# Kernel optimization log

Measured on AMD Instinct MI355X. Metric: run time of the kernel, lower is better.

The kernel has to match this reference:

```python
import jax, jax.numpy as jnp
import numpy as np

N = 4096          # nodes
F_IN = 1386       # txt_feat_len
NHID = 1024       # per-head hidden
NHEADS = 8
CODE = 64         # code_len
LRELU_ALPHA = 0.2
NEG_INF = -9e15


def _build_adj(x):
    # F.normalize + cosine sim, threshold 0.8, sign -> {0,1}, then symmetric D^-1/2 A D^-1/2
    norm = jnp.maximum(jnp.linalg.norm(x, axis=1, keepdims=True), 1e-12)
    xn = x / norm
    sim = xn @ xn.T                                  # (N,N)
    A = (sim >= 0.8).astype(x.dtype)                 # sign after thresholding
    rowsum = A.sum(axis=1)
    r = jnp.where(rowsum > 0, rowsum ** -0.5, 0.0)
    adj = r[:, None] * A * r[None, :]                # symmetric normalized
    return jax.lax.stop_gradient(adj)                # torch code detaches x / adj is non-diff


def _gat_head(x, W, a, adj, concat):
    # x: (N,Fin), W: (Fin,H), a: (2H,1)
    H = W.shape[1]
    Wh = x @ W                                        # (N,H)
    f1 = Wh @ a[:H]                                   # (N,1)
    f2 = Wh @ a[H:]                                   # (N,1)
    e = jax.nn.leaky_relu(f1 + f2.T, LRELU_ALPHA)     # (N,N) pairwise scores
    e = jnp.where(adj > 0, e, NEG_INF)
    att = jax.nn.softmax(e, axis=1)                   # masked softmax (dropout off: eval)
    h = att @ Wh                                      # (N,H)
    return jax.nn.elu(h) if concat else h


def setup_inputs() -> dict:
    key = jax.random.key(0)
    k = jax.random.split(key, 5)
    x = jax.random.normal(k[0], (N, F_IN), dtype=jnp.float32)
    s_in = 1.0 / np.sqrt(F_IN)
    W_att = jax.random.uniform(k[1], (NHEADS, F_IN, NHID), jnp.float32, -s_in, s_in)
    a_att = jax.random.uniform(k[2], (NHEADS, 2 * NHID, 1), jnp.float32, -0.1, 0.1)
    s_h = 1.0 / np.sqrt(NHEADS * NHID)
    W_out = jax.random.uniform(k[3], (NHEADS * NHID, CODE), jnp.float32, -s_h, s_h)
    a_out = jax.random.uniform(k[4], (2 * CODE, 1), jnp.float32, -0.1, 0.1)
    return {"x": x, "W_att": W_att, "a_att": a_att, "W_out": W_out, "a_out": a_out}


def reference(x, W_att, a_att, W_out, a_out):
    adj = _build_adj(x)
    # 8 concat heads, vmapped over the head axis
    heads = jax.vmap(lambda W, a: _gat_head(x, W, a, adj, True))(W_att, a_att)  # (8,N,NHID)
    h = jnp.transpose(heads, (1, 0, 2)).reshape(N, NHEADS * NHID)               # cat dim=1
    out = _gat_head(h, W_out, a_out, adj, False)                                # (N,CODE)
    code = jnp.tanh(1.0 * out)                                                   # alpha=1.0
    return code
```

## Files before the change

### kernel.cpp

```cpp
#include <hip/hip_runtime.h>
#include <hip/hip_bf16.h>
#include <stdint.h>
#include <math.h>


typedef __bf16 bf16x8 __attribute__((ext_vector_type(8)));
typedef float  f32x4  __attribute__((ext_vector_type(4)));
typedef unsigned short ushort8 __attribute__((ext_vector_type(8)));

#define AS1C(p) ((const __attribute__((address_space(1))) void*)(p))
#define AS3(p)  ((__attribute__((address_space(3))) void*)(p))

#define MODE_BF16 0
#define MODE_SIM  1
#define MODE_F32  2

__device__ __forceinline__ float bfbits2f(unsigned short u) {
    return __uint_as_float(((unsigned)u) << 16);
}
__device__ __forceinline__ unsigned short f2bfbits(float v) {
    __hip_bfloat16 b = __float2bfloat16(v);
    return *(unsigned short*)&b;
}

template<int MODE>
__device__ __forceinline__ void gemm_body(
    __hip_bfloat16* __restrict__ As, __hip_bfloat16* __restrict__ Bs,
    int bx, int by,
    const __hip_bfloat16* __restrict__ A,
    const __hip_bfloat16* __restrict__ B,
    int lda, int ldb, int K,
    void* __restrict__ Cv, int ldc, int Nreal,
    const float* __restrict__ norms,
    unsigned* __restrict__ mask,
    unsigned* __restrict__ summary)
{
    const int tid  = threadIdx.x;
    const int lane = tid & 63;
    const int wave = tid >> 6;
    const int m0   = bx * 128;
    const int n0   = by * 128;

    f32x4 acc[4][4];
#pragma unroll
    for (int i = 0; i < 4; ++i)
#pragma unroll
        for (int j = 0; j < 4; ++j)
#pragma unroll
            for (int k = 0; k < 4; ++k) acc[i][j][k] = 0.f;

    const int wm = wave >> 1, wn = wave & 1;
    const int q  = lane >> 4, ln = lane & 15;

    const int kIters = K >> 5;
    for (int kt = 0; kt < kIters; ++kt) {
        __syncthreads();
#pragma unroll
        for (int p = 0; p < 2; ++p) {
            const int t   = p * 256 + tid;
            const int row = t >> 2;
            const int kb  = (t & 3) ^ ((t >> 3) & 3);
            const __hip_bfloat16* ga = A + (long long)(m0 + row) * lda + kt * 32 + kb * 8;
            const __hip_bfloat16* gb = B + (long long)(n0 + row) * ldb + kt * 32 + kb * 8;
            __hip_bfloat16* sa = As + (p * 256 + wave * 64) * 8;
            __hip_bfloat16* sb = Bs + (p * 256 + wave * 64) * 8;
            __builtin_amdgcn_global_load_lds(AS1C(ga), AS3(sa), 16, 0, 0);
            __builtin_amdgcn_global_load_lds(AS1C(gb), AS3(sb), 16, 0, 0);
        }
        __syncthreads();

        bf16x8 afr[4], bfr[4];
#pragma unroll
        for (int rg = 0; rg < 4; ++rg) {
            const int r = wm * 64 + rg * 16 + ln;
            const int s = q ^ ((r >> 1) & 3);
            afr[rg] = *(const bf16x8*)(As + r * 32 + s * 8);
        }
#pragma unroll
        for (int cg = 0; cg < 4; ++cg) {
            const int r = wn * 64 + cg * 16 + ln;
            const int s = q ^ ((r >> 1) & 3);
            bfr[cg] = *(const bf16x8*)(Bs + r * 32 + s * 8);
        }
#pragma unroll
        for (int rg = 0; rg < 4; ++rg)
#pragma unroll
            for (int cg = 0; cg < 4; ++cg)
                acc[rg][cg] = __builtin_amdgcn_mfma_f32_16x16x32_bf16(
                    afr[rg], bfr[cg], acc[rg][cg], 0, 0, 0);
    }

#pragma unroll
    for (int rg = 0; rg < 4; ++rg) {
#pragma unroll
        for (int cg = 0; cg < 4; ++cg) {
#pragma unroll
            for (int i = 0; i < 4; ++i) {
                const int row = m0 + wm * 64 + rg * 16 + q * 4 + i;
                const int col = n0 + wn * 64 + cg * 16 + ln;
                const float v = acc[rg][cg][i];
                if (MODE == MODE_BF16) {
                    __hip_bfloat16* C = (__hip_bfloat16*)Cv;
                    C[(long long)row * ldc + col] = __float2bfloat16(v);
                } else if (MODE == MODE_SIM) {
                    if (v >= 0.8f * norms[row] * norms[col]) {
                        atomicOr(&mask[row * 128 + (col >> 5)], 1u << (col & 31));
                        atomicOr(&summary[row * 4 + (col >> 10)], 1u << ((col >> 5) & 31));
                        atomicOr(&mask[col * 128 + (row >> 5)], 1u << (row & 31));
                        atomicOr(&summary[col * 4 + (row >> 10)], 1u << ((row >> 5) & 31));
                    }
                } else {
                    if (col < Nreal) {
                        float* C = (float*)Cv;
                        C[(long long)row * ldc + col] = v;
                    }
                }
            }
        }
    }
}

__global__ __launch_bounds__(256)
void prestage(const float* __restrict__ x,
              const float* __restrict__ W_att,
              const float* __restrict__ W_out,
              const float* __restrict__ a_att,
              __hip_bfloat16* __restrict__ x_bf,
              float* __restrict__ norms,
              __hip_bfloat16* __restrict__ Wt_bf,
              __hip_bfloat16* __restrict__ WoutT,
              float* __restrict__ wa)
{
    __shared__ float ts[32][33];
    __shared__ float red[4];
    const int id  = blockIdx.x;
    const int tid = threadIdx.x;

    if (id < 4096) {
        const int i = id;
        float ss = 0.f;
        for (int c = tid; c < 1408; c += 256) {
            float v = (c < 1386) ? x[(long long)i * 1386 + c] : 0.f;
            x_bf[(long long)i * 1408 + c] = __float2bfloat16(v);
            ss += v * v;
        }
        for (int off = 32; off; off >>= 1) ss += __shfl_down(ss, off);
        if ((tid & 63) == 0) red[tid >> 6] = ss;
        __syncthreads();
        if (tid == 0) norms[i] = fmaxf(sqrtf(red[0] + red[1] + red[2] + red[3]), 1e-12f);
        return;
    }
    if (id < 16384) {
        const float* s; __hip_bfloat16* d;
        int K, N, Kpad, Npad, k0, n0;
        if (id < 15360) {
            const int b = id - 4096;
            const int h = b / 1408, r = b % 1408;
            const int kx = r % 44, ny = r / 44;
            s = W_att + (long long)h * 1386 * 1024;
            d = Wt_bf + (long long)h * 1024 * 1408;
            K = 1386; N = 1024; Kpad = 1408; Npad = 1024;
            k0 = kx * 32; n0 = ny * 32;
        } else {
            const int r = id - 15360;
            s = W_out; d = WoutT;
            K = 8192; N = 64; Kpad = 8192; Npad = 128;
            k0 = (r & 255) * 32; n0 = (r >> 8) * 32;
        }
        const int tx = tid & 31, ty = tid >> 5;
#pragma unroll
        for (int i = 0; i < 4; ++i) {
            const int k = k0 + ty + i * 8;
            const int n = n0 + tx;
            ts[ty + i * 8][tx] = (k < K && n < N) ? s[(long long)k * N + n] : 0.f;
        }
        __syncthreads();
#pragma unroll
        for (int i = 0; i < 4; ++i) {
            const int n  = n0 + ty + i * 8;
            const int kk = k0 + tx;
            if (n < Npad && kk < Kpad)
                d[(long long)n * Kpad + kk] = __float2bfloat16(ts[tx][ty + i * 8]);
        }
        return;
    }
    {
        const int b = id - 16384;
        const int h = b / 352, r = b % 352;
        const int wave = tid >> 6, lane = tid & 63;
        const int c = r * 4 + wave;
        float s1 = 0.f, s2 = 0.f;
        if (c < 1386) {
            const float* wr = W_att + ((long long)h * 1386 + c) * 1024;
            const float* a1 = a_att + (long long)h * 2048;
            const float* a2 = a1 + 1024;
#pragma unroll
            for (int t = 0; t < 16; ++t) {
                const int j = lane + t * 64;
                const float w = wr[j];
                s1 += w * a1[j];
                s2 += w * a2[j];
            }
        }
        for (int off = 32; off; off >>= 1) { s1 += __shfl_down(s1, off); s2 += __shfl_down(s2, off); }
        if (lane == 0) {
            wa[(h * 2 + 0) * 1408 + c] = s1;
            wa[(h * 2 + 1) * 1408 + c] = s2;
        }
    }
}

__global__ __launch_bounds__(256, 2)
void mega_gemm(const __hip_bfloat16* __restrict__ x_bf,
               const __hip_bfloat16* __restrict__ Wt_bf,
               __hip_bfloat16* __restrict__ Wh,
               const float* __restrict__ norms,
               unsigned* __restrict__ mask,
               unsigned* __restrict__ summ,
               const float* __restrict__ x,
               const float* __restrict__ wa,
               float2* __restrict__ f12)
{
    __shared__ __align__(16) __hip_bfloat16 As[128 * 32];
    __shared__ __align__(16) __hip_bfloat16 Bs[128 * 32];
    const int id = blockIdx.x;

    if (id < 528) {
        int t = (int)((sqrtf(8.f * id + 1.f) - 1.f) * 0.5f);
        while (t * (t + 1) / 2 > id) --t;
        while ((t + 1) * (t + 2) / 2 <= id) ++t;
        const int by = t, bx = id - t * (t + 1) / 2;
        gemm_body<MODE_SIM>(As, Bs, bx, by, x_bf, x_bf, 1408, 1408, 1408,
                            nullptr, 0, 0, norms, mask, summ);
        return;
    }
    if (id < 2576) {
        const int b  = id - 528;
        const int z  = b >> 8;
        const int r  = b & 255;
        const int bx = r & 31, by = r >> 5;
        gemm_body<MODE_BF16>(As, Bs, bx, by,
                             x_bf, Wt_bf + (long long)z * 1024 * 1408,
                             1408, 1408, 1408,
                             Wh + (long long)z * 4096 * 1024, 1024, 1024,
                             nullptr, nullptr, nullptr);
        return;
    }
    {
        const int b    = id - 2576;
        const int wave = threadIdx.x >> 6, lane = threadIdx.x & 63;
        const int i    = b * 4 + wave;
        float s[16];
#pragma unroll
        for (int j = 0; j < 16; ++j) s[j] = 0.f;
        const float* xr = x + (long long)i * 1386;
        for (int c = lane; c < 1386; c += 64) {
            const float v = xr[c];
#pragma unroll
            for (int j = 0; j < 16; ++j) s[j] += v * wa[j * 1408 + c];
        }
#pragma unroll
        for (int j = 0; j < 16; ++j)
            for (int off = 32; off; off >>= 1) s[j] += __shfl_down(s[j], off);
        if (lane == 0) {
#pragma unroll
            for (int h = 0; h < 8; ++h)
                f12[(long long)h * 4096 + i] = make_float2(s[h * 2], s[h * 2 + 1]);
        }
    }
}

__global__ __launch_bounds__(256, 2)
void out_gemm(const __hip_bfloat16* __restrict__ hout,
              const __hip_bfloat16* __restrict__ WoutT,
              float* __restrict__ parts)
{
    __shared__ __align__(16) __hip_bfloat16 As[128 * 32];
    __shared__ __align__(16) __hip_bfloat16 Bs[128 * 32];
    const int z = blockIdx.z;
    gemm_body<MODE_F32>(As, Bs, blockIdx.x, 0,
                        hout + z * 512, WoutT + z * 512, 8192, 8192, 512,
                        parts + (long long)z * 4096 * 64, 64, 64,
                        nullptr, nullptr, nullptr);
}

__global__ __launch_bounds__(256)
void attn_head(const __hip_bfloat16* __restrict__ Wh,
               const float2* __restrict__ f12,
               const unsigned* __restrict__ mask,
               const unsigned* __restrict__ summary,
               __hip_bfloat16* __restrict__ hout)
{
    const int wv   = threadIdx.x >> 6;
    const int lane = threadIdx.x & 63;
    const int i    = blockIdx.x * 4 + wv;
    const int h    = blockIdx.y;
    const float2* f = f12 + (long long)h * 4096;
    const float f1 = f[i].x;
    const unsigned* mrow = mask + (long long)i * 128;
    const __hip_bfloat16* WhH = Wh + (long long)h * 4096 * 1024;
    const uint4 sm = *(const uint4*)(summary + (long long)i * 4);
    unsigned sw[4] = { sm.x, sm.y, sm.z, sm.w };
    const int cbase = lane * 16;

    float m = -INFINITY, l = 0.f;
    float acc[16];
#pragma unroll
    for (int k = 0; k < 16; ++k) acc[k] = 0.f;

#pragma unroll
    for (int s = 0; s < 4; ++s) {
        unsigned sb = sw[s];
        while (sb) {
            const int w = s * 32 + __builtin_ctz(sb);
            sb &= sb - 1;
            unsigned bits = mrow[w];
            while (bits) {
                const int j = w * 32 + __builtin_ctz(bits);
                bits &= bits - 1;
                float e = f1 + f[j].y;
                e = e > 0.f ? e : 0.2f * e;
                float wgt;
                if (e > m) {
                    const float sc = __expf(m - e);
                    l *= sc;
#pragma unroll
                    for (int k = 0; k < 16; ++k) acc[k] *= sc;
                    m = e; wgt = 1.f;
                } else {
                    wgt = __expf(e - m);
                }
                l += wgt;
                const ushort8* p = (const ushort8*)(WhH + (long long)j * 1024 + cbase);
                const ushort8 w0 = p[0], w1 = p[1];
#pragma unroll
                for (int k = 0; k < 8; ++k) acc[k]     += wgt * bfbits2f(w0[k]);
#pragma unroll
                for (int k = 0; k < 8; ++k) acc[k + 8] += wgt * bfbits2f(w1[k]);
            }
        }
    }
    const float inv = 1.f / l;
    ushort8 o0, o1;
#pragma unroll
    for (int k = 0; k < 8; ++k) {
        float v = acc[k] * inv;     v = v > 0.f ? v : (__expf(v) - 1.f); o0[k] = f2bfbits(v);
        float u = acc[k + 8] * inv; u = u > 0.f ? u : (__expf(u) - 1.f); o1[k] = f2bfbits(u);
    }
    ushort8* op = (ushort8*)(hout + (long long)i * 8192 + (long long)h * 1024 + cbase);
    op[0] = o0; op[1] = o1;
}

__global__ void out_reduce_f(const float* __restrict__ parts,
                             const float* __restrict__ a_out,
                             float* __restrict__ Cout,
                             float* __restrict__ f1o,
                             float* __restrict__ f2o)
{
    const int i = blockIdx.x, c = threadIdx.x;
    float v = 0.f;
#pragma unroll
    for (int z = 0; z < 16; ++z) v += parts[(long long)z * 4096 * 64 + (long long)i * 64 + c];
    Cout[(long long)i * 64 + c] = v;
    float s1 = v * a_out[c];
    float s2 = v * a_out[64 + c];
    for (int off = 32; off; off >>= 1) { s1 += __shfl_down(s1, off); s2 += __shfl_down(s2, off); }
    if (c == 0) { f1o[i] = s1; f2o[i] = s2; }
}

__global__ __launch_bounds__(256)
void attn_out(const float* __restrict__ Cout,
              const float* __restrict__ f1o,
              const float* __restrict__ f2o,
              const unsigned* __restrict__ mask,
              const unsigned* __restrict__ summary,
              float* __restrict__ out)
{
    const int wv = threadIdx.x >> 6;
    const int c  = threadIdx.x & 63;
    const int i  = blockIdx.x * 4 + wv;
    const float f1 = f1o[i];
    const unsigned* mrow = mask + (long long)i * 128;
    const uint4 sm = *(const uint4*)(summary + (long long)i * 4);
    unsigned sw[4] = { sm.x, sm.y, sm.z, sm.w };
    float m = -INFINITY, l = 0.f, acc = 0.f;
#pragma unroll
    for (int s = 0; s < 4; ++s) {
        unsigned sb = sw[s];
        while (sb) {
            const int w = s * 32 + __builtin_ctz(sb);
            sb &= sb - 1;
            unsigned bits = mrow[w];
            while (bits) {
                const int j = w * 32 + __builtin_ctz(bits);
                bits &= bits - 1;
                float e = f1 + f2o[j];
                e = e > 0.f ? e : 0.2f * e;
                float wgt;
                if (e > m) { const float sc = __expf(m - e); l *= sc; acc *= sc; m = e; wgt = 1.f; }
                else       { wgt = __expf(e - m); }
                l += wgt;
                acc += wgt * Cout[(long long)j * 64 + c];
            }
        }
    }
    out[(long long)i * 64 + c] = tanhf(acc / l);
}

extern "C" void kernel_launch(void* const* d_in, const int* in_sizes, int n_in,
                              void* d_out, int out_size, void* d_ws, size_t ws_size,
                              hipStream_t stream)
{
    (void)in_sizes; (void)n_in; (void)out_size;
    const float* x     = (const float*)d_in[0];
    const float* W_att = (const float*)d_in[1];
    const float* a_att = (const float*)d_in[2];
    const float* W_out = (const float*)d_in[3];
    const float* a_out = (const float*)d_in[4];
    float* out = (float*)d_out;

    char* ws = (char*)d_ws;
    size_t off = 0;
    auto alloc = [&](size_t bytes) -> void* {
        void* p = ws + off;
        off += (bytes + 255) & ~(size_t)255;
        return p;
    };

    __hip_bfloat16* x_bf  = (__hip_bfloat16*)alloc(4096LL * 1408 * 2);
    __hip_bfloat16* Wt_bf = (__hip_bfloat16*)alloc(8LL * 1024 * 1408 * 2);
    __hip_bfloat16* WoutT = (__hip_bfloat16*)alloc(128LL * 8192 * 2);
    float*          norms = (float*)alloc(4096 * 4);
    unsigned*       mask  = (unsigned*)alloc(4096LL * 128 * 4);
    unsigned*       summ  = (unsigned*)alloc(4096LL * 4 * 4);
    float*          wa    = (float*)alloc(16LL * 1408 * 4);
    float2*         f12   = (float2*)alloc(8LL * 4096 * 8);
    float*          parts = (float*)alloc(16LL * 4096 * 64 * 4);
    float*          Cout  = (float*)alloc(4096LL * 64 * 4);
    float*          f1o   = (float*)alloc(4096 * 4);
    float*          f2o   = (float*)alloc(4096 * 4);
    __hip_bfloat16* Wh    = (__hip_bfloat16*)alloc(8LL * 4096 * 1024 * 2);
    __hip_bfloat16* hout  = (__hip_bfloat16*)alloc(8LL * 4096 * 1024 * 2);
    if (off > ws_size) return;

    hipMemsetAsync(mask, 0, 4096LL * 128 * 4 + 4096LL * 4 * 4, stream);

    prestage<<<19200, 256, 0, stream>>>(x, W_att, W_out, a_att,
                                        x_bf, norms, Wt_bf, WoutT, wa);

    mega_gemm<<<3600, 256, 0, stream>>>(x_bf, Wt_bf, Wh, norms, mask, summ,
                                        x, wa, f12);

    attn_head<<<dim3(1024, 8), 256, 0, stream>>>(Wh, f12, mask, summ, hout);

    out_gemm<<<dim3(32, 1, 16), 256, 0, stream>>>(hout, WoutT, parts);

    out_reduce_f<<<4096, 64, 0, stream>>>(parts, a_out, Cout, f1o, f2o);
    attn_out<<<1024, 256, 0, stream>>>(Cout, f1o, f2o, mask, summ, out);
}
```

Before: 326.3 us.

## Fuse ELU into Wh GEMM epilogue for self-loop-only rows and skip attention

Adds a per-row check for whether a node's adjacency holds only its own self-loop. For those rows the masked softmax puts all its weight on the node itself, so the head output is simply ELU(Wh). The Wh GEMM epilogue now writes that directly into hout, and the attention kernel exits early for such rows. This requires splitting the combined GEMM launch so the similarity mask is complete before the Wh GEMM runs, which costs extra launch serialization and per-row mask reads in the epilogue.

```diff
diff --git a/kernel.cpp b/kernel.cpp
--- a/kernel.cpp
+++ b/kernel.cpp
@@ -11,9 +11,9 @@
 #define AS1C(p) ((const __attribute__((address_space(1))) void*)(p))
 #define AS3(p)  ((__attribute__((address_space(3))) void*)(p))
 
-#define MODE_BF16 0
-#define MODE_SIM  1
-#define MODE_F32  2
+#define MODE_WH  0
+#define MODE_SIM 1
+#define MODE_F32 2
 
 __device__ __forceinline__ float bfbits2f(unsigned short u) {
     return __uint_as_float(((unsigned)u) << 16);
@@ -21,6 +21,19 @@
 __device__ __forceinline__ unsigned short f2bfbits(float v) {
     __hip_bfloat16 b = __float2bfloat16(v);
     return *(unsigned short*)&b;
+}
+
+__device__ __forceinline__ bool row_fast(const unsigned* __restrict__ mask,
+                                         const unsigned* __restrict__ summ,
+                                         int row)
+{
+    const uint4 s = *(const uint4*)(summ + row * 4);
+    unsigned sw[4] = { s.x, s.y, s.z, s.w };
+    const int wi = row >> 5;
+    bool fast = (sw[wi >> 5] == (1u << (wi & 31)));
+    sw[wi >> 5] = 0;
+    fast = fast && !(sw[0] | sw[1] | sw[2] | sw[3]);
+    return fast && (mask[row * 128 + wi] == (1u << (row & 31)));
 }
 
 template<int MODE>
@@ -33,7 +46,8 @@
     void* __restrict__ Cv, int ldc, int Nreal,
     const float* __restrict__ norms,
     unsigned* __restrict__ mask,
-    unsigned* __restrict__ summary)
+    unsigned* __restrict__ summary,
+    __hip_bfloat16* __restrict__ hout)
 {
     const int tid  = threadIdx.x;
     const int lane = tid & 63;
@@ -93,15 +107,22 @@
 #pragma unroll
     for (int rg = 0; rg < 4; ++rg) {
 #pragma unroll
-        for (int cg = 0; cg < 4; ++cg) {
-#pragma unroll
-            for (int i = 0; i < 4; ++i) {
-                const int row = m0 + wm * 64 + rg * 16 + q * 4 + i;
+        for (int i = 0; i < 4; ++i) {
+            const int row = m0 + wm * 64 + rg * 16 + q * 4 + i;
+            bool fast = false;
+            if (MODE == MODE_WH) fast = row_fast(mask, summary, row);
+#pragma unroll
+            for (int cg = 0; cg < 4; ++cg) {
                 const int col = n0 + wn * 64 + cg * 16 + ln;
                 const float v = acc[rg][cg][i];
-                if (MODE == MODE_BF16) {
-                    __hip_bfloat16* C = (__hip_bfloat16*)Cv;
-                    C[(long long)row * ldc + col] = __float2bfloat16(v);
+                if (MODE == MODE_WH) {
+                    if (fast) {
+                        const float u = v > 0.f ? v : (__expf(v) - 1.f);
+                        hout[(long long)row * 8192 + col] = __float2bfloat16(u);
+                    } else {
+                        __hip_bfloat16* C = (__hip_bfloat16*)Cv;
+                        C[(long long)row * ldc + col] = __float2bfloat16(v);
+                    }
                 } else if (MODE == MODE_SIM) {
                     if (v >= 0.8f * norms[row] * norms[col]) {
                         atomicOr(&mask[row * 128 + (col >> 5)], 1u << (col & 31));
@@ -211,15 +232,13 @@
 }
 
 __global__ __launch_bounds__(256, 2)
-void mega_gemm(const __hip_bfloat16* __restrict__ x_bf,
-               const __hip_bfloat16* __restrict__ Wt_bf,
-               __hip_bfloat16* __restrict__ Wh,
-               const float* __restrict__ norms,
-               unsigned* __restrict__ mask,
-               unsigned* __restrict__ summ,
-               const float* __restrict__ x,
-               const float* __restrict__ wa,
-               float2* __restrict__ f12)
+void simf12(const __hip_bfloat16* __restrict__ x_bf,
+            const float* __restrict__ norms,
+            unsigned* __restrict__ mask,
+            unsigned* __restrict__ summ,
+            const float* __restrict__ x,
+            const float* __restrict__ wa,
+            float2* __restrict__ f12)
 {
     __shared__ __align__(16) __hip_bfloat16 As[128 * 32];
     __shared__ __align__(16) __hip_bfloat16 Bs[128 * 32];
@@ -231,23 +250,11 @@
         while ((t + 1) * (t + 2) / 2 <= id) ++t;
         const int by = t, bx = id - t * (t + 1) / 2;
         gemm_body<MODE_SIM>(As, Bs, bx, by, x_bf, x_bf, 1408, 1408, 1408,
-                            nullptr, 0, 0, norms, mask, summ);
+                            nullptr, 0, 0, norms, mask, summ, nullptr);
         return;
     }
-    if (id < 2576) {
-        const int b  = id - 528;
-        const int z  = b >> 8;
-        const int r  = b & 255;
-        const int bx = r & 31, by = r >> 5;
-        gemm_body<MODE_BF16>(As, Bs, bx, by,
-                             x_bf, Wt_bf + (long long)z * 1024 * 1408,
-                             1408, 1408, 1408,
-                             Wh + (long long)z * 4096 * 1024, 1024, 1024,
-                             nullptr, nullptr, nullptr);
-        return;
-    }
     {
-        const int b    = id - 2576;
+        const int b    = id - 528;
         const int wave = threadIdx.x >> 6, lane = threadIdx.x & 63;
         const int i    = b * 4 + wave;
         float s[16];
@@ -268,6 +275,27 @@
                 f12[(long long)h * 4096 + i] = make_float2(s[h * 2], s[h * 2 + 1]);
         }
     }
+}
+
+__global__ __launch_bounds__(256, 2)
+void whh(const __hip_bfloat16* __restrict__ x_bf,
+         const __hip_bfloat16* __restrict__ Wt_bf,
+         __hip_bfloat16* __restrict__ Wh,
+         __hip_bfloat16* __restrict__ hout,
+         unsigned* __restrict__ mask,
+         unsigned* __restrict__ summ)
+{
+    __shared__ __align__(16) __hip_bfloat16 As[128 * 32];
+    __shared__ __align__(16) __hip_bfloat16 Bs[128 * 32];
+    const int id = blockIdx.x;
+    const int z  = id >> 8;
+    const int r  = id & 255;
+    const int bx = r & 31, by = r >> 5;
+    gemm_body<MODE_WH>(As, Bs, bx, by,
+                       x_bf, Wt_bf + (long long)z * 1024 * 1408,
+                       1408, 1408, 1408,
+                       Wh + (long long)z * 4096 * 1024, 1024, 1024,
+                       nullptr, mask, summ, hout + (long long)z * 1024);
 }
 
 __global__ __launch_bounds__(256, 2)
@@ -281,20 +309,22 @@
     gemm_body<MODE_F32>(As, Bs, blockIdx.x, 0,
                         hout + z * 512, WoutT + z * 512, 8192, 8192, 512,
                         parts + (long long)z * 4096 * 64, 64, 64,
-                        nullptr, nullptr, nullptr);
+                        nullptr, nullptr, nullptr, nullptr);
 }
 
 __global__ __launch_bounds__(256)
-void attn_head(const __hip_bfloat16* __restrict__ Wh,
-               const float2* __restrict__ f12,
-               const unsigned* __restrict__ mask,
-               const unsigned* __restrict__ summary,
-               __hip_bfloat16* __restrict__ hout)
+void attn_fix(const __hip_bfloat16* __restrict__ Wh,
+              const float2* __restrict__ f12,
+              const unsigned* __restrict__ mask,
+              const unsigned* __restrict__ summary,
+              __hip_bfloat16* __restrict__ hout)
 {
     const int wv   = threadIdx.x >> 6;
     const int lane = threadIdx.x & 63;
     const int i    = blockIdx.x * 4 + wv;
     const int h    = blockIdx.y;
+    if (row_fast(mask, summary, i)) return;
+
     const float2* f = f12 + (long long)h * 4096;
     const float f1 = f[i].x;
     const unsigned* mrow = mask + (long long)i * 128;
@@ -448,10 +478,11 @@
     prestage<<<19200, 256, 0, stream>>>(x, W_att, W_out, a_att,
                                         x_bf, norms, Wt_bf, WoutT, wa);
 
-    mega_gemm<<<3600, 256, 0, stream>>>(x_bf, Wt_bf, Wh, norms, mask, summ,
-                                        x, wa, f12);
-
-    attn_head<<<dim3(1024, 8), 256, 0, stream>>>(Wh, f12, mask, summ, hout);
+    simf12<<<1552, 256, 0, stream>>>(x_bf, norms, mask, summ, x, wa, f12);
+
+    whh<<<2048, 256, 0, stream>>>(x_bf, Wt_bf, Wh, hout, mask, summ);
+
+    attn_fix<<<dim3(1024, 8), 256, 0, stream>>>(Wh, f12, mask, summ, hout);
 
     out_gemm<<<dim3(32, 1, 16), 256, 0, stream>>>(hout, WoutT, parts);
 
```

Measured after the change: 332.5 us. No clear change (+1.9%).
